# Kernel tuning notes

Measured on AMD Instinct MI355X. Metric: run time of the kernel, lower is better.

Reference implementation:

```python
import jax, jax.numpy as jnp
import numpy as np

B, T, S = 4, 1024, 1024
E, H, D, M = 768, 12, 64, 3072
SCALE = 1.0 / (D ** 0.5)
EPS = 1e-5


def setup_inputs() -> dict:
    key = jax.random.key(0)
    ks = jax.random.split(key, 20)
    s = 0.02

    def n(k, shp):
        return jax.random.normal(k, shp, jnp.float32) * s

    return {
        "target": jax.random.normal(ks[0], (B, T, E), jnp.float32),
        "memory": jax.random.normal(ks[1], (B, S, E), jnp.float32),
        # self-attention: per-head Q/K/V projections stacked over heads [H,E,D]
        "sa_wq": n(ks[2], (H, E, D)), "sa_bq": jnp.zeros((H, D), jnp.float32),
        "sa_wk": n(ks[3], (H, E, D)), "sa_bk": jnp.zeros((H, D), jnp.float32),
        "sa_wv": n(ks[4], (H, E, D)), "sa_bv": jnp.zeros((H, D), jnp.float32),
        "sa_wo": n(ks[5], (H * D, E)), "sa_bo": jnp.zeros((E,), jnp.float32),
        # cross-attention
        "ca_wq": n(ks[6], (H, E, D)), "ca_bq": jnp.zeros((H, D), jnp.float32),
        "ca_wk": n(ks[7], (H, E, D)), "ca_bk": jnp.zeros((H, D), jnp.float32),
        "ca_wv": n(ks[8], (H, E, D)), "ca_bv": jnp.zeros((H, D), jnp.float32),
        "ca_wo": n(ks[9], (H * D, E)), "ca_bo": jnp.zeros((E,), jnp.float32),
        # layernorms
        "ln1_g": jnp.ones((E,), jnp.float32), "ln1_b": jnp.zeros((E,), jnp.float32),
        "ln2_g": jnp.ones((E,), jnp.float32), "ln2_b": jnp.zeros((E,), jnp.float32),
        "ln3_g": jnp.ones((E,), jnp.float32), "ln3_b": jnp.zeros((E,), jnp.float32),
        # FFN
        "ffn_w1": n(ks[10], (E, M)), "ffn_b1": jnp.zeros((M,), jnp.float32),
        "ffn_w2": n(ks[11], (M, E)), "ffn_b2": jnp.zeros((E,), jnp.float32),
    }


def layernorm(x, g, b):
    mu = jnp.mean(x, axis=-1, keepdims=True)
    var = jnp.mean(jnp.square(x - mu), axis=-1, keepdims=True)
    return (x - mu) * jax.lax.rsqrt(var + EPS) * g + b


def mha(q_in, k_in, v_in, wq, bq, wk, bk, wv, bv, wo, bo, mask=None):
    # batched equivalent of the per-head looped projections
    Q = jnp.einsum('bse,hed->bhsd', q_in, wq) + bq[None, :, None, :]
    K = jnp.einsum('bte,hed->bhtd', k_in, wk) + bk[None, :, None, :]
    V = jnp.einsum('bte,hed->bhtd', v_in, wv) + bv[None, :, None, :]
    scores = jnp.einsum('bhsd,bhtd->bhst', Q, K) * SCALE
    if mask is not None:
        scores = jnp.where(mask, scores, -jnp.inf)
    w = jax.nn.softmax(scores, axis=-1)
    o = jnp.einsum('bhst,bhtd->bhsd', w, V)  # [B,H,Sq,D]
    o = o.transpose(0, 2, 1, 3).reshape(q_in.shape[0], q_in.shape[1], H * D)
    return o @ wo + bo


def reference(target, memory,
              sa_wq, sa_bq, sa_wk, sa_bk, sa_wv, sa_bv, sa_wo, sa_bo,
              ca_wq, ca_bq, ca_wk, ca_bk, ca_wv, ca_bv, ca_wo, ca_bo,
              ln1_g, ln1_b, ln2_g, ln2_b, ln3_g, ln3_b,
              ffn_w1, ffn_b1, ffn_w2, ffn_b2):
    Tq = target.shape[1]
    causal = jnp.tril(jnp.ones((Tq, Tq), bool))  # [T,T], broadcasts over B,H
    # pre-norm self-attention + residual
    x = layernorm(target, ln1_g, ln1_b)
    x = mha(x, x, x, sa_wq, sa_bq, sa_wk, sa_bk, sa_wv, sa_bv, sa_wo, sa_bo, causal) + target
    # pre-norm cross-attention + residual
    res = x
    y = layernorm(x, ln2_g, ln2_b)
    x = mha(y, memory, memory, ca_wq, ca_bq, ca_wk, ca_bk, ca_wv, ca_bv, ca_wo, ca_bo) + res
    # pre-norm FFN (Linear -> GELU -> Linear) + residual
    res = x
    y = layernorm(x, ln3_g, ln3_b)
    x = jax.nn.gelu(y @ ffn_w1 + ffn_b1) @ ffn_w2 + ffn_b2 + res
    return x
```

## Files before the change

kernel.cpp:

```cpp
#include <hip/hip_runtime.h>
#include <hip/hip_bf16.h>
#include <stdint.h>

#define BB 4
#define TT 1024
#define SS 1024
#define EE 768
#define HH 12
#define DDIM 64
#define MM 3072
#define NROWS 4096
#define ATT_SCALE 0.125f

typedef unsigned short u16;
using short8 = __attribute__((ext_vector_type(8))) short;
using f32x4  = __attribute__((ext_vector_type(4))) float;

__device__ inline f32x4 mfma16(short8 a, short8 b, f32x4 c) {
  return __builtin_amdgcn_mfma_f32_16x16x32_bf16(a, b, c, 0, 0, 0);
}

__device__ inline float b2f(u16 u) {
  union { uint32_t i; float f; } z; z.i = ((uint32_t)u) << 16; return z.f;
}
__device__ inline u16 f2b(float f) {
  __hip_bfloat16 h = __float2bfloat16(f);
  return *reinterpret_cast<u16*>(&h);
}
__device__ inline float loadf(const float* p) { return *p; }
__device__ inline float loadf(const u16* p) { return b2f(*p); }

__device__ inline float gelu_f(float x) {
  const float k0 = 0.7978845608028654f;
  const float k1 = 0.044715f;
  float t = tanhf(k0 * (x + k1 * x * x * x));
  return 0.5f * x * (1.0f + t);
}

__device__ inline void gload16(const u16* g, u16* l) {
  __builtin_amdgcn_global_load_lds(
      (const __attribute__((address_space(1))) unsigned int*)g,
      (__attribute__((address_space(3))) unsigned int*)l, 16, 0, 0);
}

__global__ void transpose_k(const float* __restrict__ in, u16* __restrict__ out,
                            int R, int C) {
  __shared__ u16 tile[32][34];
  int bz = blockIdx.z;
  const float* ip = in + (size_t)bz * R * C;
  u16* op = out + (size_t)bz * R * C;
  int r0 = blockIdx.y * 32, c0 = blockIdx.x * 32;
  int tx = threadIdx.x, ty = threadIdx.y;
#pragma unroll
  for (int j = 0; j < 32; j += 8)
    tile[ty + j][tx] = f2b(ip[(size_t)(r0 + ty + j) * C + (c0 + tx)]);
  __syncthreads();
#pragma unroll
  for (int j = 0; j < 32; j += 8)
    op[(size_t)(c0 + ty + j) * R + (r0 + tx)] = tile[tx][ty + j];
}

__global__ void transpose3_k(const float* __restrict__ s0,
                             const float* __restrict__ s1,
                             const float* __restrict__ s2,
                             u16* __restrict__ out) {
  __shared__ u16 tile[32][34];
  int bz = blockIdx.z;
  int src = bz / HH, head = bz % HH;
  const float* in = (src == 0) ? s0 : (src == 1) ? s1 : s2;
  const float* ip = in + (size_t)head * EE * DDIM;
  u16* op = out + (size_t)bz * EE * DDIM;
  int r0 = blockIdx.y * 32, c0 = blockIdx.x * 32;
  int tx = threadIdx.x, ty = threadIdx.y;
#pragma unroll
  for (int j = 0; j < 32; j += 8)
    tile[ty + j][tx] = f2b(ip[(size_t)(r0 + ty + j) * DDIM + (c0 + tx)]);
  __syncthreads();
#pragma unroll
  for (int j = 0; j < 32; j += 8)
    op[(size_t)(c0 + ty + j) * EE + (r0 + tx)] = tile[tx][ty + j];
}

__global__ void transpose2_k(const float* __restrict__ s0,
                             const float* __restrict__ s1,
                             u16* __restrict__ out) {
  __shared__ u16 tile[32][34];
  int bz = blockIdx.z;
  const float* ip = (bz == 0) ? s0 : s1;
  u16* op = out + (size_t)bz * EE * EE;
  int r0 = blockIdx.y * 32, c0 = blockIdx.x * 32;
  int tx = threadIdx.x, ty = threadIdx.y;
#pragma unroll
  for (int j = 0; j < 32; j += 8)
    tile[ty + j][tx] = f2b(ip[(size_t)(r0 + ty + j) * EE + (c0 + tx)]);
  __syncthreads();
#pragma unroll
  for (int j = 0; j < 32; j += 8)
    op[(size_t)(c0 + ty + j) * EE + (r0 + tx)] = tile[tx][ty + j];
}

__global__ void tr_v2_k(const u16* __restrict__ in0, int ld0, size_t bs0,
                        u16* __restrict__ out0,
                        const u16* __restrict__ in1, int ld1, size_t bs1,
                        u16* __restrict__ out1) {
  __shared__ u16 tile[32][34];
  int z = blockIdx.z;
  const u16* in; u16* out; int ldi; size_t bstride; int bz;
  if (z < 48) { in = in0; out = out0; ldi = ld0; bstride = bs0; bz = z; }
  else        { in = in1; out = out1; ldi = ld1; bstride = bs1; bz = z - 48; }
  const u16* ip = in + (size_t)(bz / HH) * bstride + (size_t)(bz % HH) * DDIM;
  u16* op = out + (size_t)bz * DDIM * SS;
  int r0 = blockIdx.y * 32, c0 = blockIdx.x * 32;
  int tx = threadIdx.x, ty = threadIdx.y;
#pragma unroll
  for (int j = 0; j < 32; j += 8)
    tile[ty + j][tx] = ip[(size_t)(r0 + ty + j) * ldi + (c0 + tx)];
  __syncthreads();
#pragma unroll
  for (int j = 0; j < 32; j += 8)
    op[(size_t)(c0 + ty + j) * SS + (r0 + tx)] = tile[tx][ty + j];
}

__global__ __launch_bounds__(256) void prologue_misc_k(
    const float* __restrict__ mem, u16* __restrict__ memB,
    const float* __restrict__ a3, const float* __restrict__ b3,
    const float* __restrict__ c3, float* __restrict__ d3,
    const float* __restrict__ a2, const float* __restrict__ b2,
    float* __restrict__ d2) {
  int blk = blockIdx.x, t = threadIdx.x;
  if (blk < 3072) {
    int i = (blk * 256 + t) * 4;
    float4 f = *(const float4*)(mem + i);
    u16 o[4] = {f2b(f.x), f2b(f.y), f2b(f.z), f2b(f.w)};
    *(uint64_t*)(memB + i) = *(const uint64_t*)o;
  } else if (blk < 3081) {
    int i = (blk - 3072) * 256 + t;
    if (i < 768) d3[i] = a3[i];
    else if (i < 1536) d3[i] = b3[i - 768];
    else d3[i] = c3[i - 1536];
  } else {
    int i = (blk - 3081) * 256 + t;
    if (i < 768) d2[i] = a2[i];
    else d2[i] = b2[i - 768];
  }
}

template <typename T>
__global__ __launch_bounds__(256) void layernorm_k(const T* __restrict__ x,
    const float* __restrict__ g, const float* __restrict__ b,
    u16* __restrict__ y) {
  int row = blockIdx.x, t = threadIdx.x;
  const T* xr = x + (size_t)row * EE;
  float v0 = loadf(xr + t), v1 = loadf(xr + t + 256), v2 = loadf(xr + t + 512);
  float s = v0 + v1 + v2;
#pragma unroll
  for (int m = 32; m >= 1; m >>= 1) s += __shfl_xor(s, m);
  __shared__ float red[8];
  int wv = t >> 6, ln = t & 63;
  if (ln == 0) red[wv] = s;
  __syncthreads();
  float mean = (red[0] + red[1] + red[2] + red[3]) * (1.0f / EE);
  float d0 = v0 - mean, d1 = v1 - mean, d2 = v2 - mean;
  float s2 = d0 * d0 + d1 * d1 + d2 * d2;
#pragma unroll
  for (int m = 32; m >= 1; m >>= 1) s2 += __shfl_xor(s2, m);
  if (ln == 0) red[4 + wv] = s2;
  __syncthreads();
  float var = (red[4] + red[5] + red[6] + red[7]) * (1.0f / EE);
  float rstd = rsqrtf(var + 1e-5f);
  u16* yr = y + (size_t)row * EE;
  yr[t]       = f2b(d0 * rstd * g[t]       + b[t]);
  yr[t + 256] = f2b(d1 * rstd * g[t + 256] + b[t + 256]);
  yr[t + 512] = f2b(d2 * rstd * g[t + 512] + b[t + 512]);
}

template <int RESMODE, bool GELU, bool XCDSWZ, typename OutT>
__global__ __launch_bounds__(256) void gemm128_k(
    const u16* __restrict__ A, const u16* __restrict__ Bt,
    const float* __restrict__ bias, const void* __restrict__ res,
    OutT* __restrict__ C, int M, int N, int K) {
  __shared__ u16 As[2][128 * 32];
  __shared__ u16 Bs[2][128 * 32];
  int bx = blockIdx.x, by = blockIdx.y;
  if (XCDSWZ) {
    const int nbx = N >> 7;
    int id = bx + nbx * by;
    int per = (nbx * (M >> 7)) >> 3;
    int sid = (id & 7) * per + (id >> 3);
    bx = sid % nbx; by = sid / nbx;
  }
  const int bm = by * 128, bn = bx * 128;
  const int t = threadIdx.x;
  const int wave = t >> 6, lane = t & 63;
  const int wr = wave >> 1, wc = wave & 1;
  const int g = lane >> 4, li = lane & 15;
  f32x4 acc[4][4] = {};
  const size_t rowskip = (size_t)64 * K;
  const int scol = (((t & 3) ^ ((t >> 3) & 3)) * 8);
  const u16* Ag = A + (size_t)(bm + (t >> 2)) * K + scol;
  const u16* Bg = Bt + (size_t)(bn + (t >> 2)) * K + scol;

  gload16(Ag, &As[0][t * 8]);
  gload16(Ag + rowskip, &As[0][2048 + t * 8]);
  gload16(Bg, &Bs[0][t * 8]);
  gload16(Bg + rowskip, &Bs[0][2048 + t * 8]);
  __syncthreads();

  const int nsteps = K >> 5;
  for (int s = 0; s < nsteps; s++) {
    const int cur = s & 1;
    if (s + 1 < nsteps) {
      const int k0 = (s + 1) << 5;
      gload16(Ag + k0, &As[cur ^ 1][t * 8]);
      gload16(Ag + rowskip + k0, &As[cur ^ 1][2048 + t * 8]);
      gload16(Bg + k0, &Bs[cur ^ 1][t * 8]);
      gload16(Bg + rowskip + k0, &Bs[cur ^ 1][2048 + t * 8]);
    }
    short8 af[4], bf[4];
#pragma unroll
    for (int i = 0; i < 4; i++) {
      const int ar = wr * 64 + i * 16 + li;
      af[i] = *(const short8*)(&As[cur][ar * 32 + ((g ^ ((ar >> 1) & 3)) * 8)]);
      const int br = wc * 64 + i * 16 + li;
      bf[i] = *(const short8*)(&Bs[cur][br * 32 + ((g ^ ((br >> 1) & 3)) * 8)]);
    }
#pragma unroll
    for (int mi = 0; mi < 4; mi++)
#pragma unroll
      for (int nj = 0; nj < 4; nj++)
        acc[mi][nj] = mfma16(af[mi], bf[nj], acc[mi][nj]);
    __syncthreads();
  }

#pragma unroll
  for (int mi = 0; mi < 4; mi++)
#pragma unroll
    for (int nj = 0; nj < 4; nj++) {
      int n = bn + wc * 64 + nj * 16 + li;
      float bv = bias[n];
#pragma unroll
      for (int i = 0; i < 4; i++) {
        int m = bm + wr * 64 + mi * 16 + g * 4 + i;
        float val = acc[mi][nj][i] + bv;
        if (GELU) val = gelu_f(val);
        if (RESMODE == 1) val += ((const float*)res)[(size_t)m * N + n];
        else if (RESMODE == 2) val += b2f(((const u16*)res)[(size_t)m * N + n]);
        if constexpr (sizeof(OutT) == 2) C[(size_t)m * N + n] = f2b(val);
        else                             C[(size_t)m * N + n] = val;
      }
    }
}

__global__ __launch_bounds__(256) void gemm128_dual_k(
    const u16* __restrict__ A0, const u16* __restrict__ B0,
    const float* __restrict__ bias0, u16* __restrict__ C0, int N0, int nbx0,
    const u16* __restrict__ A1, const u16* __restrict__ B1,
    const float* __restrict__ bias1, u16* __restrict__ C1, int N1,
    int M, int K) {
  __shared__ u16 As[2][128 * 32];
  __shared__ u16 Bs[2][128 * 32];
  const int id = blockIdx.x + 30 * blockIdx.y;
  const int sid = (id & 7) * 120 + (id >> 3);
  const int x = sid % 30, y = sid / 30;
  const bool p1 = (x >= nbx0);
  const u16* A = p1 ? A1 : A0;
  const u16* Bt = p1 ? B1 : B0;
  const float* bias = p1 ? bias1 : bias0;
  u16* C = p1 ? C1 : C0;
  const int N = p1 ? N1 : N0;
  const int bn = (p1 ? x - nbx0 : x) * 128;
  const int bm = y * 128;
  const int t = threadIdx.x;
  const int wave = t >> 6, lane = t & 63;
  const int wr = wave >> 1, wc = wave & 1;
  const int g = lane >> 4, li = lane & 15;
  f32x4 acc[4][4] = {};
  const size_t rowskip = (size_t)64 * K;
  const int scol = (((t & 3) ^ ((t >> 3) & 3)) * 8);
  const u16* Ag = A + (size_t)(bm + (t >> 2)) * K + scol;
  const u16* Bg = Bt + (size_t)(bn + (t >> 2)) * K + scol;

  gload16(Ag, &As[0][t * 8]);
  gload16(Ag + rowskip, &As[0][2048 + t * 8]);
  gload16(Bg, &Bs[0][t * 8]);
  gload16(Bg + rowskip, &Bs[0][2048 + t * 8]);
  __syncthreads();

  const int nsteps = K >> 5;
  for (int s = 0; s < nsteps; s++) {
    const int cur = s & 1;
    if (s + 1 < nsteps) {
      const int k0 = (s + 1) << 5;
      gload16(Ag + k0, &As[cur ^ 1][t * 8]);
      gload16(Ag + rowskip + k0, &As[cur ^ 1][2048 + t * 8]);
      gload16(Bg + k0, &Bs[cur ^ 1][t * 8]);
      gload16(Bg + rowskip + k0, &Bs[cur ^ 1][2048 + t * 8]);
    }
    short8 af[4], bf[4];
#pragma unroll
    for (int i = 0; i < 4; i++) {
      const int ar = wr * 64 + i * 16 + li;
      af[i] = *(const short8*)(&As[cur][ar * 32 + ((g ^ ((ar >> 1) & 3)) * 8)]);
      const int br = wc * 64 + i * 16 + li;
      bf[i] = *(const short8*)(&Bs[cur][br * 32 + ((g ^ ((br >> 1) & 3)) * 8)]);
    }
#pragma unroll
    for (int mi = 0; mi < 4; mi++)
#pragma unroll
      for (int nj = 0; nj < 4; nj++)
        acc[mi][nj] = mfma16(af[mi], bf[nj], acc[mi][nj]);
    __syncthreads();
  }

#pragma unroll
  for (int mi = 0; mi < 4; mi++)
#pragma unroll
    for (int nj = 0; nj < 4; nj++) {
      int n = bn + wc * 64 + nj * 16 + li;
      float bv = bias[n];
#pragma unroll
      for (int i = 0; i < 4; i++) {
        int m = bm + wr * 64 + mi * 16 + g * 4 + i;
        C[(size_t)m * N + n] = f2b(acc[mi][nj][i] + bv);
      }
    }
}

template <int RESMODE, bool GELU, bool XCDSWZ, typename OutT>
__global__ __launch_bounds__(256) void gemm64_k(
    const u16* __restrict__ A, const u16* __restrict__ Bt,
    const float* __restrict__ bias, const void* __restrict__ res,
    OutT* __restrict__ C, int M, int N, int K) {
  __shared__ u16 As[2][64 * 64];
  __shared__ u16 Bs[2][64 * 64];
  int bx = blockIdx.x, by = blockIdx.y;
  if (XCDSWZ) {
    const int nbx = N >> 6;
    int id = bx + nbx * by;
    int per = (nbx * (M >> 6)) >> 3;
    int sid = (id & 7) * per + (id >> 3);
    bx = sid % nbx; by = sid / nbx;
  }
  const int bm = by * 64, bn = bx * 64;
  const int t = threadIdx.x;
  const int wave = t >> 6, lane = t & 63;
  const int wr = wave >> 1, wc = wave & 1;
  const int g = lane >> 4, li = lane & 15;
  f32x4 acc[2][2] = {};
  const int srow = t >> 3;
  const int scolz = ((t & 7) * 8) ^ ((srow & 7) << 3);
  const size_t skip32 = (size_t)32 * K;
  const u16* Ag = A + (size_t)(bm + srow) * K + scolz;
  const u16* Bg = Bt + (size_t)(bn + srow) * K + scolz;

  gload16(Ag, &As[0][t * 8]);
  gload16(Ag + skip32, &As[0][2048 + t * 8]);
  gload16(Bg, &Bs[0][t * 8]);
  gload16(Bg + skip32, &Bs[0][2048 + t * 8]);
  __syncthreads();

  const int nsteps = K >> 6;
  for (int s = 0; s < nsteps; s++) {
    const int cur = s & 1;
    if (s + 1 < nsteps) {
      const int k0 = (s + 1) << 6;
      gload16(Ag + k0, &As[cur ^ 1][t * 8]);
      gload16(Ag + skip32 + k0, &As[cur ^ 1][2048 + t * 8]);
      gload16(Bg + k0, &Bs[cur ^ 1][t * 8]);
      gload16(Bg + skip32 + k0, &Bs[cur ^ 1][2048 + t * 8]);
    }
    short8 af[2][2], bf[2][2];
#pragma unroll
    for (int mt = 0; mt < 2; mt++)
#pragma unroll
      for (int kk = 0; kk < 2; kk++) {
        int ar = wr * 32 + mt * 16 + li;
        af[mt][kk] = *(const short8*)(&As[cur][ar * 64 + ((kk * 32 + g * 8) ^ ((ar & 7) << 3))]);
        int br = wc * 32 + mt * 16 + li;
        bf[mt][kk] = *(const short8*)(&Bs[cur][br * 64 + ((kk * 32 + g * 8) ^ ((br & 7) << 3))]);
      }
#pragma unroll
    for (int mt = 0; mt < 2; mt++)
#pragma unroll
      for (int nt = 0; nt < 2; nt++)
#pragma unroll
        for (int kk = 0; kk < 2; kk++)
          acc[mt][nt] = mfma16(af[mt][kk], bf[nt][kk], acc[mt][nt]);
    __syncthreads();
  }

#pragma unroll
  for (int mt = 0; mt < 2; mt++)
#pragma unroll
    for (int nt = 0; nt < 2; nt++) {
      int n = bn + wc * 32 + nt * 16 + li;
      float bv = bias[n];
#pragma unroll
      for (int i = 0; i < 4; i++) {
        int m = bm + wr * 32 + mt * 16 + g * 4 + i;
        float val = acc[mt][nt][i] + bv;
        if (GELU) val = gelu_f(val);
        if (RESMODE == 1) val += ((const float*)res)[(size_t)m * N + n];
        else if (RESMODE == 2) val += b2f(((const u16*)res)[(size_t)m * N + n]);
        if constexpr (sizeof(OutT) == 2) C[(size_t)m * N + n] = f2b(val);
        else                             C[(size_t)m * N + n] = val;
      }
    }
}

template <bool CAUSAL>
__global__ __launch_bounds__(256) void attn4_k(
    const u16* __restrict__ Q, const u16* __restrict__ K,
    const u16* __restrict__ VT, u16* __restrict__ O,
    int ldq, int ldk) {
  int b, h, q0;
  if (CAUSAL) {
    int id = blockIdx.x;
    int cu = id & 255, slot = id >> 8;
    int q, hb;
    if (cu < 96) {
      int p = cu & 1, r = cu >> 1;
      q = (slot == 0 ? 0 : slot == 1 ? 6 : 14) + p;
      hb = r;
    } else if (cu < 192) {
      int c2 = cu - 96; int p = c2 & 1, r = c2 >> 1;
      q = (slot == 0 ? 2 : slot == 1 ? 8 : 12) + p;
      hb = r;
    } else if (cu < 224) {
      int c2 = cu - 192;
      int p = c2 & 1, r = c2 >> 1;
      if (slot == 0)      { q = 10;    hb = c2; }
      else if (slot == 1) { q = 11;    hb = c2; }
      else                { q = 4 + p; hb = r; }
    } else {
      int c2 = cu - 224;
      int p = c2 & 1, r = c2 >> 1;
      if (slot == 0)      { q = 4;      hb = 16 + c2; }
      else if (slot == 1) { q = 5;      hb = 16 + c2; }
      else                { q = 10 + p; hb = 32 + r; }
    }
    h = hb % HH; b = hb / HH; q0 = q * 64;
  } else {
    b = blockIdx.z; h = blockIdx.y; q0 = blockIdx.x * 64;
  }
  int tid = threadIdx.x, wave = tid >> 6, lane = tid & 63;
  int g = lane >> 4, li = lane & 15;
  const u16* Qb = Q + (size_t)b * TT * ldq + h * DDIM;
  const u16* Kb = K + (size_t)b * SS * ldk + h * DDIM;
  const u16* Vb = VT + (size_t)(b * HH + h) * DDIM * SS;
  u16* Ob = O + (size_t)b * TT * EE + h * DDIM;

  __shared__ u16 Ks[128 * 64];
  __shared__ u16 Vs[64 * 128];
  __shared__ u16 Ps[4][16][132];

  int qrow = q0 + wave * 16 + li;
  short8 qf0 = *(const short8*)(Qb + (size_t)qrow * ldq + g * 8);
  short8 qf1 = *(const short8*)(Qb + (size_t)qrow * ldq + 32 + g * 8);

  f32x4 accO[4] = {};
  float lrow[4] = {0.f, 0.f, 0.f, 0.f};

  const int krow = tid >> 3;
  const int vrow = tid >> 4;
  const int qmax = q0 + wave * 16 + 15;

  int kvEnd = CAUSAL ? (((q0 + 64 + 127) >> 7) << 7) : SS;
  for (int kv0 = 0; kv0 < kvEnd; kv0 += 128) {
#pragma unroll
    for (int j = 0; j < 4; j++) {
      int kr = j * 32 + krow;
      int kc = ((tid & 7) * 8) ^ ((kr & 7) << 3);
      gload16(Kb + (size_t)(kv0 + kr) * ldk + kc, &Ks[j * 2048 + tid * 8]);
    }
#pragma unroll
    for (int j = 0; j < 4; j++) {
      int vr = j * 16 + vrow;
      int vc = ((tid & 15) * 8) ^ ((vr & 15) << 3);
      gload16(Vb + (size_t)vr * SS + kv0 + vc, &Vs[j * 2048 + tid * 8]);
    }
    __syncthreads();

    if (!CAUSAL || kv0 <= qmax) {
      const bool needMask = CAUSAL && (kv0 + 127 > qmax);
      f32x4 s[8];
#pragma unroll
      for (int kt = 0; kt < 8; kt++) {
        int kr = kt * 16 + li;
        int sw = (kr & 7) << 3;
        short8 kf0 = *(const short8*)(&Ks[kr * 64 + ((g * 8) ^ sw)]);
        short8 kf1 = *(const short8*)(&Ks[kr * 64 + ((g * 8 + 32) ^ sw)]);
        f32x4 z = {};
        z = mfma16(qf0, kf0, z);
        z = mfma16(qf1, kf1, z);
        s[kt] = z;
      }

      float rsum[4] = {0.f, 0.f, 0.f, 0.f};
#pragma unroll
      for (int kt = 0; kt < 8; kt++)
#pragma unroll
        for (int i = 0; i < 4; i++) {
          float sv = s[kt][i] * ATT_SCALE;
          if (needMask) {
            int qi = q0 + wave * 16 + g * 4 + i;
            int ti = kv0 + kt * 16 + li;
            if (ti > qi) sv = -1e30f;
          }
          float p = __expf(sv);
          s[kt][i] = p;
          rsum[i] += p;
        }
#pragma unroll
      for (int msk = 1; msk < 16; msk <<= 1)
#pragma unroll
        for (int i = 0; i < 4; i++) rsum[i] += __shfl_xor(rsum[i], msk);
#pragma unroll
      for (int i = 0; i < 4; i++) lrow[i] += rsum[i];

#pragma unroll
      for (int kt = 0; kt < 8; kt++)
#pragma unroll
        for (int i = 0; i < 4; i++)
          Ps[wave][g * 4 + i][kt * 16 + li] = f2b(s[kt][i]);

#pragma unroll
      for (int tc = 0; tc < 4; tc++) {
        short8 pf = *(const short8*)(&Ps[wave][li][tc * 32 + g * 8]);
#pragma unroll
        for (int dt = 0; dt < 4; dt++) {
          int vr = dt * 16 + li;
          short8 vf = *(const short8*)(&Vs[vr * 128 + ((tc * 32 + g * 8) ^ ((vr & 15) << 3))]);
          accO[dt] = mfma16(pf, vf, accO[dt]);
        }
      }
    }
    __syncthreads();
  }

#pragma unroll
  for (int i = 0; i < 4; i++) {
    float inv = 1.0f / lrow[i];
    int q = q0 + wave * 16 + g * 4 + i;
#pragma unroll
    for (int dt = 0; dt < 4; dt++)
      Ob[(size_t)q * EE + dt * 16 + li] = f2b(accO[dt][i] * inv);
  }
}

static inline void* wsoff(void* ws, size_t& off, size_t bytes) {
  void* p = (char*)ws + off;
  off += (bytes + 255) & ~(size_t)255;
  return p;
}

extern "C" void kernel_launch(void* const* d_in, const int* in_sizes, int n_in,
                              void* d_out, int out_size, void* d_ws, size_t ws_size,
                              hipStream_t stream) {
  const float* target = (const float*)d_in[0];
  const float* memory = (const float*)d_in[1];
  const float* sa_wq = (const float*)d_in[2];  const float* sa_bq = (const float*)d_in[3];
  const float* sa_wk = (const float*)d_in[4];  const float* sa_bk = (const float*)d_in[5];
  const float* sa_wv = (const float*)d_in[6];  const float* sa_bv = (const float*)d_in[7];
  const float* sa_wo = (const float*)d_in[8];  const float* sa_bo = (const float*)d_in[9];
  const float* ca_wq = (const float*)d_in[10]; const float* ca_bq = (const float*)d_in[11];
  const float* ca_wk = (const float*)d_in[12]; const float* ca_bk = (const float*)d_in[13];
  const float* ca_wv = (const float*)d_in[14]; const float* ca_bv = (const float*)d_in[15];
  const float* ca_wo = (const float*)d_in[16]; const float* ca_bo = (const float*)d_in[17];
  const float* ln1_g = (const float*)d_in[18]; const float* ln1_b = (const float*)d_in[19];
  const float* ln2_g = (const float*)d_in[20]; const float* ln2_b = (const float*)d_in[21];
  const float* ln3_g = (const float*)d_in[22]; const float* ln3_b = (const float*)d_in[23];
  const float* ffn_w1 = (const float*)d_in[24]; const float* ffn_b1 = (const float*)d_in[25];
  const float* ffn_w2 = (const float*)d_in[26]; const float* ffn_b2 = (const float*)d_in[27];

  size_t off = 0;
  const size_t WB = (size_t)EE * EE * 2;
  u16* wqkvT_sa = (u16*)wsoff(d_ws, off, 3 * WB);
  u16* wqT_ca   = (u16*)wsoff(d_ws, off, WB);
  u16* wkvT_ca  = (u16*)wsoff(d_ws, off, 2 * WB);
  u16* woT_sa   = (u16*)wsoff(d_ws, off, WB);
  u16* woT_ca   = (u16*)wsoff(d_ws, off, WB);
  u16* w1T      = (u16*)wsoff(d_ws, off, (size_t)EE * MM * 2);
  u16* w2T      = (u16*)wsoff(d_ws, off, (size_t)EE * MM * 2);
  float* bsa_qkv = (float*)wsoff(d_ws, off, 2304 * 4);
  float* bca_kv  = (float*)wsoff(d_ws, off, 1536 * 4);
  const size_t AB = (size_t)NROWS * EE * 2;
  u16* mx2   = (u16*)wsoff(d_ws, off, AB);
  u16* lnb   = (u16*)wsoff(d_ws, off, AB);
  u16* S2    = (u16*)wsoff(d_ws, off, 3 * AB);
  u16* S3    = (u16*)wsoff(d_ws, off, AB);
  u16* x1    = (u16*)wsoff(d_ws, off, AB);
  u16* vtsa  = (u16*)wsoff(d_ws, off, AB);
  u16* vtca  = (u16*)wsoff(d_ws, off, AB);
  u16* kvca  = (u16*)wsoff(d_ws, off, 2 * AB);
  u16* qkv_sa = S2;
  u16* qb_ca  = S2;
  u16* attn_out = S3;
  u16* f1     = S2;
  u16* memB   = mx2;
  u16* x2     = mx2;

  dim3 tb(32, 8);
  transpose3_k<<<dim3(2, 24, 36), tb, 0, stream>>>(sa_wq, sa_wk, sa_wv, wqkvT_sa);
  transpose3_k<<<dim3(2, 24, 36), tb, 0, stream>>>(ca_wq, ca_wk, ca_wv, wqT_ca);
  transpose2_k<<<dim3(24, 24, 2), tb, 0, stream>>>(sa_wo, ca_wo, woT_sa);
  transpose_k<<<dim3(96, 24, 1), tb, 0, stream>>>(ffn_w1, w1T, EE, MM);
  transpose_k<<<dim3(24, 96, 1), tb, 0, stream>>>(ffn_w2, w2T, MM, EE);
  prologue_misc_k<<<3087, 256, 0, stream>>>(memory, memB,
      sa_bq, sa_bk, sa_bv, bsa_qkv, ca_bk, ca_bv, bca_kv);

  layernorm_k<float><<<NROWS, 256, 0, stream>>>(target, ln1_g, ln1_b, lnb);
  gemm128_dual_k<<<dim3(30, 32), 256, 0, stream>>>(
      lnb, wqkvT_sa, bsa_qkv, qkv_sa, 3 * EE, 18,
      memB, wkvT_ca, bca_kv, kvca, 2 * EE, NROWS, EE);
  tr_v2_k<<<dim3(2, 32, 96), tb, 0, stream>>>(
      qkv_sa + 2 * EE, 3 * EE, (size_t)TT * 3 * EE, vtsa,
      kvca + EE, 2 * EE, (size_t)SS * 2 * EE, vtca);

  attn4_k<true><<<dim3(768, 1, 1), 256, 0, stream>>>(
      qkv_sa, qkv_sa + EE, vtsa, attn_out, 3 * EE, 3 * EE);
  gemm64_k<1, false, true, u16><<<dim3(12, 64), 256, 0, stream>>>(
      attn_out, woT_sa, sa_bo, target, x1, NROWS, EE, EE);

  layernorm_k<u16><<<NROWS, 256, 0, stream>>>(x1, ln2_g, ln2_b, lnb);
  gemm64_k<0, false, true, u16><<<dim3(12, 64), 256, 0, stream>>>(
      lnb, wqT_ca, ca_bq, nullptr, qb_ca, NROWS, EE, EE);
  attn4_k<false><<<dim3(16, 12, 4), 256, 0, stream>>>(
      qb_ca, kvca, vtca, attn_out, EE, 2 * EE);
  gemm64_k<2, false, true, u16><<<dim3(12, 64), 256, 0, stream>>>(
      attn_out, woT_ca, ca_bo, x1, x2, NROWS, EE, EE);

  layernorm_k<u16><<<NROWS, 256, 0, stream>>>(x2, ln3_g, ln3_b, lnb);
  gemm128_k<0, true, true, u16><<<dim3(24, 32), 256, 0, stream>>>(
      lnb, w1T, ffn_b1, nullptr, f1, NROWS, MM, EE);
  gemm64_k<2, false, true, float><<<dim3(12, 64), 256, 0, stream>>>(
      f1, w2T, ffn_b2, x2, (float*)d_out, NROWS, EE, MM);
}
```

Baseline: 250.6 us.

## Merge prologue kernels into one launch and fuse V-transpose into QKV GEMM epilogue

Replaces five weight-transpose kernels, the misc prologue and the first layernorm with a single prep_k launch whose block index selects the task. The separate V-transpose kernel is removed: the dual QKV/KV GEMM epilogue now also writes the V columns in transposed per-head layout using 8-byte stores. This cuts launch overhead and one full read/write pass over V, at the cost of extra scattered stores in the GEMM epilogue and a heterogeneous large grid.

Result: faster. 235.2 us (-6.1%).

```diff
diff --git a/kernel.cpp b/kernel.cpp
--- a/kernel.cpp
+++ b/kernel.cpp
@@ -43,105 +43,99 @@
       (__attribute__((address_space(3))) unsigned int*)l, 16, 0, 0);
 }
 
-__global__ void transpose_k(const float* __restrict__ in, u16* __restrict__ out,
-                            int R, int C) {
+__global__ __launch_bounds__(256) void prep_k(
+    const float* __restrict__ target, const float* __restrict__ ln1_g,
+    const float* __restrict__ ln1_b, u16* __restrict__ lnb,
+    const float* __restrict__ mem, u16* __restrict__ memB,
+    const float* __restrict__ bq3, const float* __restrict__ bk3,
+    const float* __restrict__ bv3, float* __restrict__ d3,
+    const float* __restrict__ bk2, const float* __restrict__ bv2,
+    float* __restrict__ d2,
+    const float* __restrict__ sa_wq, const float* __restrict__ sa_wk,
+    const float* __restrict__ sa_wv, u16* __restrict__ wqkvT_sa,
+    const float* __restrict__ ca_wq, const float* __restrict__ ca_wk,
+    const float* __restrict__ ca_wv, u16* __restrict__ wqkvT_ca,
+    const float* __restrict__ sa_wo, const float* __restrict__ ca_wo,
+    u16* __restrict__ woT,
+    const float* __restrict__ ffn_w1, u16* __restrict__ w1T,
+    const float* __restrict__ ffn_w2, u16* __restrict__ w2T) {
   __shared__ u16 tile[32][34];
-  int bz = blockIdx.z;
-  const float* ip = in + (size_t)bz * R * C;
-  u16* op = out + (size_t)bz * R * C;
-  int r0 = blockIdx.y * 32, c0 = blockIdx.x * 32;
-  int tx = threadIdx.x, ty = threadIdx.y;
-#pragma unroll
-  for (int j = 0; j < 32; j += 8)
-    tile[ty + j][tx] = f2b(ip[(size_t)(r0 + ty + j) * C + (c0 + tx)]);
-  __syncthreads();
-#pragma unroll
-  for (int j = 0; j < 32; j += 8)
-    op[(size_t)(c0 + ty + j) * R + (r0 + tx)] = tile[tx][ty + j];
-}
-
-__global__ void transpose3_k(const float* __restrict__ s0,
-                             const float* __restrict__ s1,
-                             const float* __restrict__ s2,
-                             u16* __restrict__ out) {
-  __shared__ u16 tile[32][34];
-  int bz = blockIdx.z;
-  int src = bz / HH, head = bz % HH;
-  const float* in = (src == 0) ? s0 : (src == 1) ? s1 : s2;
-  const float* ip = in + (size_t)head * EE * DDIM;
-  u16* op = out + (size_t)bz * EE * DDIM;
-  int r0 = blockIdx.y * 32, c0 = blockIdx.x * 32;
-  int tx = threadIdx.x, ty = threadIdx.y;
-#pragma unroll
-  for (int j = 0; j < 32; j += 8)
-    tile[ty + j][tx] = f2b(ip[(size_t)(r0 + ty + j) * DDIM + (c0 + tx)]);
-  __syncthreads();
-#pragma unroll
-  for (int j = 0; j < 32; j += 8)
-    op[(size_t)(c0 + ty + j) * EE + (r0 + tx)] = tile[tx][ty + j];
-}
-
-__global__ void transpose2_k(const float* __restrict__ s0,
-                             const float* __restrict__ s1,
-                             u16* __restrict__ out) {
-  __shared__ u16 tile[32][34];
-  int bz = blockIdx.z;
-  const float* ip = (bz == 0) ? s0 : s1;
-  u16* op = out + (size_t)bz * EE * EE;
-  int r0 = blockIdx.y * 32, c0 = blockIdx.x * 32;
-  int tx = threadIdx.x, ty = threadIdx.y;
-#pragma unroll
-  for (int j = 0; j < 32; j += 8)
-    tile[ty + j][tx] = f2b(ip[(size_t)(r0 + ty + j) * EE + (c0 + tx)]);
-  __syncthreads();
-#pragma unroll
-  for (int j = 0; j < 32; j += 8)
-    op[(size_t)(c0 + ty + j) * EE + (r0 + tx)] = tile[tx][ty + j];
-}
-
-__global__ void tr_v2_k(const u16* __restrict__ in0, int ld0, size_t bs0,
-                        u16* __restrict__ out0,
-                        const u16* __restrict__ in1, int ld1, size_t bs1,
-                        u16* __restrict__ out1) {
-  __shared__ u16 tile[32][34];
-  int z = blockIdx.z;
-  const u16* in; u16* out; int ldi; size_t bstride; int bz;
-  if (z < 48) { in = in0; out = out0; ldi = ld0; bstride = bs0; bz = z; }
-  else        { in = in1; out = out1; ldi = ld1; bstride = bs1; bz = z - 48; }
-  const u16* ip = in + (size_t)(bz / HH) * bstride + (size_t)(bz % HH) * DDIM;
-  u16* op = out + (size_t)bz * DDIM * SS;
-  int r0 = blockIdx.y * 32, c0 = blockIdx.x * 32;
-  int tx = threadIdx.x, ty = threadIdx.y;
-#pragma unroll
-  for (int j = 0; j < 32; j += 8)
-    tile[ty + j][tx] = ip[(size_t)(r0 + ty + j) * ldi + (c0 + tx)];
-  __syncthreads();
-#pragma unroll
-  for (int j = 0; j < 32; j += 8)
-    op[(size_t)(c0 + ty + j) * SS + (r0 + tx)] = tile[tx][ty + j];
-}
-
-__global__ __launch_bounds__(256) void prologue_misc_k(
-    const float* __restrict__ mem, u16* __restrict__ memB,
-    const float* __restrict__ a3, const float* __restrict__ b3,
-    const float* __restrict__ c3, float* __restrict__ d3,
-    const float* __restrict__ a2, const float* __restrict__ b2,
-    float* __restrict__ d2) {
-  int blk = blockIdx.x, t = threadIdx.x;
-  if (blk < 3072) {
-    int i = (blk * 256 + t) * 4;
+  __shared__ float red[8];
+  const int blk = blockIdx.x, t = threadIdx.x;
+  if (blk < 4096) {
+    const float* xr = target + (size_t)blk * EE;
+    float v0 = xr[t], v1 = xr[t + 256], v2 = xr[t + 512];
+    float s = v0 + v1 + v2;
+#pragma unroll
+    for (int m = 32; m >= 1; m >>= 1) s += __shfl_xor(s, m);
+    int wv = t >> 6, ln = t & 63;
+    if (ln == 0) red[wv] = s;
+    __syncthreads();
+    float mean = (red[0] + red[1] + red[2] + red[3]) * (1.0f / EE);
+    float e0 = v0 - mean, e1 = v1 - mean, e2 = v2 - mean;
+    float s2 = e0 * e0 + e1 * e1 + e2 * e2;
+#pragma unroll
+    for (int m = 32; m >= 1; m >>= 1) s2 += __shfl_xor(s2, m);
+    if (ln == 0) red[4 + wv] = s2;
+    __syncthreads();
+    float var = (red[4] + red[5] + red[6] + red[7]) * (1.0f / EE);
+    float rstd = rsqrtf(var + 1e-5f);
+    u16* yr = lnb + (size_t)blk * EE;
+    yr[t]       = f2b(e0 * rstd * ln1_g[t]       + ln1_b[t]);
+    yr[t + 256] = f2b(e1 * rstd * ln1_g[t + 256] + ln1_b[t + 256]);
+    yr[t + 512] = f2b(e2 * rstd * ln1_g[t + 512] + ln1_b[t + 512]);
+  } else if (blk < 7168) {
+    int i = ((blk - 4096) * 256 + t) * 4;
     float4 f = *(const float4*)(mem + i);
     u16 o[4] = {f2b(f.x), f2b(f.y), f2b(f.z), f2b(f.w)};
     *(uint64_t*)(memB + i) = *(const uint64_t*)o;
-  } else if (blk < 3081) {
-    int i = (blk - 3072) * 256 + t;
-    if (i < 768) d3[i] = a3[i];
-    else if (i < 1536) d3[i] = b3[i - 768];
-    else d3[i] = c3[i - 1536];
+  } else if (blk < 7177) {
+    int i = (blk - 7168) * 256 + t;
+    if (i < 768) d3[i] = bq3[i];
+    else if (i < 1536) d3[i] = bk3[i - 768];
+    else d3[i] = bv3[i - 1536];
+  } else if (blk < 7183) {
+    int i = (blk - 7177) * 256 + t;
+    if (i < 768) d2[i] = bk2[i];
+    else d2[i] = bv2[i - 768];
   } else {
-    int i = (blk - 3081) * 256 + t;
-    if (i < 768) d2[i] = a2[i];
-    else d2[i] = b2[i - 768];
+    const float* ip; u16* op; int R, C, bx, by;
+    int r = blk - 7183;
+    if (r < 1728) {
+      int u = r / 48, rr = r % 48; bx = rr & 1; by = rr >> 1;
+      const float* s = (u < 12) ? sa_wq : (u < 24) ? sa_wk : sa_wv;
+      ip = s + (size_t)(u % 12) * EE * DDIM;
+      op = wqkvT_sa + (size_t)u * EE * DDIM;
+      R = EE; C = DDIM;
+    } else if (r < 3456) {
+      r -= 1728;
+      int u = r / 48, rr = r % 48; bx = rr & 1; by = rr >> 1;
+      const float* s = (u < 12) ? ca_wq : (u < 24) ? ca_wk : ca_wv;
+      ip = s + (size_t)(u % 12) * EE * DDIM;
+      op = wqkvT_ca + (size_t)u * EE * DDIM;
+      R = EE; C = DDIM;
+    } else if (r < 4608) {
+      r -= 3456;
+      int u = r / 576, rr = r % 576; bx = rr % 24; by = rr / 24;
+      ip = (u == 0) ? sa_wo : ca_wo;
+      op = woT + (size_t)u * EE * EE;
+      R = EE; C = EE;
+    } else if (r < 6912) {
+      r -= 4608; bx = r % 96; by = r / 96;
+      ip = ffn_w1; op = w1T; R = EE; C = MM;
+    } else {
+      r -= 6912; bx = r % 24; by = r / 24;
+      ip = ffn_w2; op = w2T; R = MM; C = EE;
+    }
+    int r0 = by * 32, c0 = bx * 32;
+    int tx = t & 31, ty = t >> 5;
+#pragma unroll
+    for (int j = 0; j < 32; j += 8)
+      tile[ty + j][tx] = f2b(ip[(size_t)(r0 + ty + j) * C + (c0 + tx)]);
+    __syncthreads();
+#pragma unroll
+    for (int j = 0; j < 32; j += 8)
+      op[(size_t)(c0 + ty + j) * R + (r0 + tx)] = tile[tx][ty + j];
   }
 }
 
@@ -256,6 +250,7 @@
     const float* __restrict__ bias0, u16* __restrict__ C0, int N0, int nbx0,
     const u16* __restrict__ A1, const u16* __restrict__ B1,
     const float* __restrict__ bias1, u16* __restrict__ C1, int N1,
+    u16* __restrict__ vtsa, u16* __restrict__ vtca,
     int M, int K) {
   __shared__ u16 As[2][128 * 32];
   __shared__ u16 Bs[2][128 * 32];
@@ -312,16 +307,30 @@
     __syncthreads();
   }
 
+  const int vbase = p1 ? 768 : 1536;
+  u16* vtX = p1 ? vtca : vtsa;
+  const bool isVblk = (bn >= vbase);
+
 #pragma unroll
   for (int mi = 0; mi < 4; mi++)
 #pragma unroll
     for (int nj = 0; nj < 4; nj++) {
       int n = bn + wc * 64 + nj * 16 + li;
       float bv = bias[n];
+      u16 vv[4];
 #pragma unroll
       for (int i = 0; i < 4; i++) {
         int m = bm + wr * 64 + mi * 16 + g * 4 + i;
-        C[(size_t)m * N + n] = f2b(acc[mi][nj][i] + bv);
+        u16 o = f2b(acc[mi][nj][i] + bv);
+        C[(size_t)m * N + n] = o;
+        vv[i] = o;
+      }
+      if (isVblk) {
+        int hd = n - vbase;
+        int m0 = bm + wr * 64 + mi * 16 + g * 4;
+        int bb = m0 >> 10, t0 = m0 & 1023;
+        *(uint64_t*)(&vtX[((size_t)(bb * HH + (hd >> 6)) << 16) +
+                          ((size_t)(hd & 63) << 10) + t0]) = *(const uint64_t*)vv;
       }
     }
 }
@@ -600,22 +609,19 @@
   u16* memB   = mx2;
   u16* x2     = mx2;
 
-  dim3 tb(32, 8);
-  transpose3_k<<<dim3(2, 24, 36), tb, 0, stream>>>(sa_wq, sa_wk, sa_wv, wqkvT_sa);
-  transpose3_k<<<dim3(2, 24, 36), tb, 0, stream>>>(ca_wq, ca_wk, ca_wv, wqT_ca);
-  transpose2_k<<<dim3(24, 24, 2), tb, 0, stream>>>(sa_wo, ca_wo, woT_sa);
-  transpose_k<<<dim3(96, 24, 1), tb, 0, stream>>>(ffn_w1, w1T, EE, MM);
-  transpose_k<<<dim3(24, 96, 1), tb, 0, stream>>>(ffn_w2, w2T, MM, EE);
-  prologue_misc_k<<<3087, 256, 0, stream>>>(memory, memB,
-      sa_bq, sa_bk, sa_bv, bsa_qkv, ca_bk, ca_bv, bca_kv);
-
-  layernorm_k<float><<<NROWS, 256, 0, stream>>>(target, ln1_g, ln1_b, lnb);
+  prep_k<<<16399, 256, 0, stream>>>(
+      target, ln1_g, ln1_b, lnb,
+      memory, memB,
+      sa_bq, sa_bk, sa_bv, bsa_qkv, ca_bk, ca_bv, bca_kv,
+      sa_wq, sa_wk, sa_wv, wqkvT_sa,
+      ca_wq, ca_wk, ca_wv, wqT_ca,
+      sa_wo, ca_wo, woT_sa,
+      ffn_w1, w1T, ffn_w2, w2T);
+
   gemm128_dual_k<<<dim3(30, 32), 256, 0, stream>>>(
       lnb, wqkvT_sa, bsa_qkv, qkv_sa, 3 * EE, 18,
-      memB, wkvT_ca, bca_kv, kvca, 2 * EE, NROWS, EE);
-  tr_v2_k<<<dim3(2, 32, 96), tb, 0, stream>>>(
-      qkv_sa + 2 * EE, 3 * EE, (size_t)TT * 3 * EE, vtsa,
-      kvca + EE, 2 * EE, (size_t)SS * 2 * EE, vtca);
+      memB, wkvT_ca, bca_kv, kvca, 2 * EE,
+      vtsa, vtca, NROWS, EE);
 
   attn4_k<true><<<dim3(768, 1, 1), 256, 0, stream>>>(
       qkv_sa, qkv_sa + EE, vtsa, attn_out, 3 * EE, 3 * EE);
```
